# Kernel tuning notes

Measured on AMD Instinct MI355X. Metric: run time of the kernel, lower is better.

## Reference

```python
import jax, jax.numpy as jnp
import numpy as np

B, S, D = 16, 2048, 2048  # S == D required for m_q + output broadcast in original code


def setup_inputs() -> dict:
    key = jax.random.key(0)
    ks = jax.random.split(key, 8)
    scale = 1.0 / np.sqrt(D)
    return {
        "hidden_list": jax.random.normal(ks[0], (B, S, D), dtype=jnp.float32),
        "m_q": jax.random.normal(ks[1], (D,), dtype=jnp.float32),
        "Wq": jax.random.normal(ks[2], (D, D), dtype=jnp.float32) * scale,
        "bq": jax.random.normal(ks[3], (D,), dtype=jnp.float32) * scale,
        "Wm": jax.random.normal(ks[4], (D, D), dtype=jnp.float32) * scale,
        "bm": jax.random.normal(ks[5], (D,), dtype=jnp.float32) * scale,
        "Wa": jax.random.normal(ks[6], (D, D), dtype=jnp.float32) * scale,
        "ba": jax.random.normal(ks[7], (D,), dtype=jnp.float32) * scale,
    }


def reference(hidden_list, m_q, Wq, bq, Wm, bm, Wa, ba):
    # hidden_list: [B, S, D]; m_q: [D]
    hq = jnp.tanh(jnp.einsum("bsd,ed->bse", hidden_list, Wq) + bq)      # [B,S,D]
    mq = jnp.tanh(Wm @ m_q + bm)                                        # [D]
    Sg = hq * mq                                                        # gated bilinear, [B,S,D]
    alpha = jax.nn.softmax(jnp.einsum("bsd,ed->bse", Sg, Wa) + ba, axis=-1)  # [B,S,D]
    output = jnp.sum(alpha * hidden_list, axis=-1)                      # [B,S]
    m_q_new = m_q + output                                              # broadcast [D]+[B,S] (S==D)
    return output, m_q_new
```

## Files before the change

kernel.cpp:

```cpp
#include <hip/hip_runtime.h>

typedef unsigned short u16;
typedef short bf16x8 __attribute__((ext_vector_type(8)));
typedef u16 u16x8 __attribute__((ext_vector_type(8)));
typedef float f32x4 __attribute__((ext_vector_type(4)));

__device__ __forceinline__ float bf2f(u16 u) {
    union { unsigned u; float f; } c; c.u = ((unsigned)u) << 16; return c.f;
}
__device__ __forceinline__ u16 f2bf(float f) {
    union { float f; unsigned u; } c; c.f = f;
    unsigned r = c.u + 0x7FFFu + ((c.u >> 16) & 1u);
    return (u16)(r >> 16);
}
__device__ __forceinline__ float tanh_fast(float x) {
    float e = __expf(2.0f * x);
    return 1.0f - 2.0f / (e + 1.0f);
}
__device__ __forceinline__ void gll16(const void* g, void* l) {
    __builtin_amdgcn_global_load_lds((const __attribute__((address_space(1))) void*)g,
                                     (__attribute__((address_space(3))) void*)l, 16, 0, 0);
}

#define BAR() do { __builtin_amdgcn_sched_barrier(0); __builtin_amdgcn_s_barrier(); \
                   __builtin_amdgcn_sched_barrier(0); } while (0)

__global__ __launch_bounds__(256) void cvt_f32_bf16(const float* __restrict__ src,
                                                    u16* __restrict__ dst, int n8) {
    int i = blockIdx.x * blockDim.x + threadIdx.x;
    int stride = gridDim.x * blockDim.x;
    for (; i < n8; i += stride) {
        const float4* s = (const float4*)(src + (size_t)i * 8);
        float4 a = s[0], b = s[1];
        u16x8 o;
        o[0] = f2bf(a.x); o[1] = f2bf(a.y); o[2] = f2bf(a.z); o[3] = f2bf(a.w);
        o[4] = f2bf(b.x); o[5] = f2bf(b.y); o[6] = f2bf(b.z); o[7] = f2bf(b.w);
        *(u16x8*)(dst + (size_t)i * 8) = o;
    }
}

__global__ __launch_bounds__(256) void mq_kernel(const float* __restrict__ Wm,
                                                 const float* __restrict__ q,
                                                 const float* __restrict__ bm,
                                                 float* __restrict__ mq, int D) {
    int w = threadIdx.x >> 6, l = threadIdx.x & 63;
    int e = blockIdx.x * 4 + w;
    const float* wp = Wm + (size_t)e * D;
    float s = 0.f;
    for (int j = 0; j < D; j += 256) {
        float4 wv = *(const float4*)(wp + j + l * 4);
        float4 qv = *(const float4*)(q + j + l * 4);
        s += wv.x * qv.x + wv.y * qv.y + wv.z * qv.z + wv.w * qv.w;
    }
    #pragma unroll
    for (int o = 32; o >= 1; o >>= 1) s += __shfl_xor(s, o);
    if (l == 0) mq[e] = tanh_fast(s + bm[e]);
}

template <int EPI>
__global__ __launch_bounds__(256, 2) void gemm8(const u16* __restrict__ A,
                                                const u16* __restrict__ B,
                                                const float* __restrict__ bias,
                                                const float* __restrict__ gate,
                                                u16* __restrict__ C,
                                                int M, int N, int K) {
    __shared__ u16 sh[32768];
    char* LDS = (char*)sh;
    const int K2 = K * 2;
    const int KT = K >> 6;

    const int tid = threadIdx.x;
    const int w = tid >> 6, l = tid & 63;
    const int wm = w >> 1, wn = w & 1;

    int orig = blockIdx.x + gridDim.x * blockIdx.y;
    int nwg = gridDim.x * gridDim.y;
    int id = ((nwg & 7) == 0) ? ((orig & 7) * (nwg >> 3) + (orig >> 3)) : orig;
    const int tileN = (id % gridDim.x) * 128;
    const int tileM = (id / gridDim.x) * 128;

    const int srow = tid >> 3;
    const int cc = ((tid & 7) ^ (srow & 7)) << 4;
    const char* srcA = (const char*)A + (size_t)(tileM + srow) * K2 + cc;
    const char* srcB = (const char*)B + (size_t)(tileN + srow) * K2 + cc;
    char* dstBase = LDS + tid * 16;
    const size_t rowStep = (size_t)32 * K2;

#define STG_A(tk) do { size_t go = (size_t)(tk) * 128; char* d = dstBase + (((tk) & 1) << 14); \
    gll16(srcA + go,               d);         gll16(srcA + go + rowStep,     d + 4096);       \
    gll16(srcA + go + 2 * rowStep, d + 8192);  gll16(srcA + go + 3 * rowStep, d + 12288); } while (0)
#define STG_B(tk) do { size_t go = (size_t)(tk) * 128; char* d = dstBase + 32768 + (((tk) & 1) << 14); \
    gll16(srcB + go,               d);         gll16(srcB + go + rowStep,     d + 4096);       \
    gll16(srcB + go + 2 * rowStep, d + 8192);  gll16(srcB + go + 3 * rowStep, d + 12288); } while (0)

    const int sw = l & 7;
    const int rowA = (wm * 64 + (l & 15)) * 128;
    const int rowB = (wn * 64 + (l & 15)) * 128;
    const int ck0 = (((l >> 4) ^ sw) << 4);
    const int ck1 = (((4 + (l >> 4)) ^ sw) << 4);
    const char* pA0 = LDS + rowA + ck0;
    const char* pA1 = LDS + rowA + ck1;
    const char* pB0 = LDS + 32768 + rowB + ck0;
    const char* pB1 = LDS + 32768 + rowB + ck1;

    f32x4 acc[4][4] = {};

    STG_A(0); STG_B(0); STG_A(1); STG_B(1);
    asm volatile("s_waitcnt vmcnt(8)" ::: "memory");
    BAR();

#define ITER(t, P) do {                                                         \
    constexpr int SA = (P) * 16384;                                             \
    bf16x8 af[4][2], bf[4][2];                                                  \
               \
    _Pragma("unroll")                                                           \
    for (int fm = 0; fm < 4; ++fm) {                                            \
        af[fm][0] = *(const bf16x8*)(pA0 + SA + fm * 2048);                     \
        af[fm][1] = *(const bf16x8*)(pA1 + SA + fm * 2048);                     \
    }                                                                           \
    _Pragma("unroll")                                                           \
    for (int fn = 0; fn < 4; ++fn) {                                            \
        bf[fn][0] = *(const bf16x8*)(pB0 + SA + fn * 2048);                     \
        bf[fn][1] = *(const bf16x8*)(pB1 + SA + fn * 2048);                     \
    }                                                                           \
    asm volatile("s_waitcnt lgkmcnt(0)" ::: "memory");                          \
    __builtin_amdgcn_sched_barrier(0);                                          \
    BAR();                                                                      \
                \
    if ((t) + 2 < KT) { STG_A((t) + 2); STG_B((t) + 2); }                       \
    __builtin_amdgcn_s_setprio(1);                                              \
    _Pragma("unroll")                                                           \
    for (int fm = 0; fm < 4; ++fm)                                              \
        _Pragma("unroll")                                                       \
        for (int fn = 0; fn < 4; ++fn) {                                        \
            acc[fm][fn] = __builtin_amdgcn_mfma_f32_16x16x32_bf16(              \
                af[fm][0], bf[fn][0], acc[fm][fn], 0, 0, 0);                    \
            acc[fm][fn] = __builtin_amdgcn_mfma_f32_16x16x32_bf16(              \
                af[fm][1], bf[fn][1], acc[fm][fn], 0, 0, 0);                    \
        }                                                                       \
    __builtin_amdgcn_s_setprio(0);                                              \
    if ((t) + 2 < KT)      asm volatile("s_waitcnt vmcnt(8)" ::: "memory");     \
    else if ((t) + 1 < KT) asm volatile("s_waitcnt vmcnt(0)" ::: "memory");     \
    BAR();                                                                      \
} while (0)

    for (int tt = 0; tt < KT; tt += 2) {
        ITER(tt, 0);
        ITER(tt + 1, 1);
    }
#undef ITER
#undef STG_A
#undef STG_B

    const int cr = (l >> 4) * 4;
    const int cl = l & 15;
    #pragma unroll
    for (int fn = 0; fn < 4; ++fn) {
        const int col = tileN + wn * 64 + fn * 16 + cl;
        const float bs = bias[col];
        float gt = 0.f;
        if (EPI == 0) gt = gate[col];
        #pragma unroll
        for (int fm = 0; fm < 4; ++fm)
            #pragma unroll
            for (int r = 0; r < 4; ++r) {
                const int row = tileM + wm * 64 + fm * 16 + cr + r;
                float v = acc[fm][fn][r] + bs;
                if (EPI == 0) v = tanh_fast(v) * gt;
                C[(size_t)row * N + col] = f2bf(v);
            }
    }
}

__global__ __launch_bounds__(256) void softmax_out(const u16* __restrict__ logits,
                                                   const float* __restrict__ hidden,
                                                   const float* __restrict__ m_q,
                                                   float* __restrict__ out,
                                                   int D, int R) {
    const int r = blockIdx.x;
    const int t = threadIdx.x;
    const int w = t >> 6, l = t & 63;
    const u16* lp = logits + (size_t)r * D + t * 8;
    const float* hp = hidden + (size_t)r * D + t * 8;

    bf16x8 lv = *(const bf16x8*)lp;
    float lf[8];
    #pragma unroll
    for (int j = 0; j < 8; ++j) lf[j] = bf2f((u16)lv[j]);
    float4 h0 = *(const float4*)hp;
    float4 h1 = *(const float4*)(hp + 4);
    float hv[8] = {h0.x, h0.y, h0.z, h0.w, h1.x, h1.y, h1.z, h1.w};

    float m = lf[0];
    #pragma unroll
    for (int j = 1; j < 8; ++j) m = fmaxf(m, lf[j]);
    #pragma unroll
    for (int o = 32; o >= 1; o >>= 1) m = fmaxf(m, __shfl_xor(m, o));

    __shared__ float red[8];
    if (l == 0) red[w] = m;
    __syncthreads();
    m = fmaxf(fmaxf(red[0], red[1]), fmaxf(red[2], red[3]));
    __syncthreads();

    float se = 0.f, sh = 0.f;
    #pragma unroll
    for (int j = 0; j < 8; ++j) {
        float e = __expf(lf[j] - m);
        se += e;
        sh += e * hv[j];
    }
    #pragma unroll
    for (int o = 32; o >= 1; o >>= 1) { se += __shfl_xor(se, o); sh += __shfl_xor(sh, o); }
    if (l == 0) { red[w] = se; red[4 + w] = sh; }
    __syncthreads();
    if (t == 0) {
        float SE = red[0] + red[1] + red[2] + red[3];
        float SH = red[4] + red[5] + red[6] + red[7];
        float o = SH / SE;
        out[r] = o;
        out[R + r] = m_q[r & (D - 1)] + o;
    }
}

extern "C" void kernel_launch(void* const* d_in, const int* in_sizes, int n_in,
                              void* d_out, int out_size, void* d_ws, size_t ws_size,
                              hipStream_t stream) {
    const float* hidden = (const float*)d_in[0];
    const float* m_q    = (const float*)d_in[1];
    const float* Wq     = (const float*)d_in[2];
    const float* bq     = (const float*)d_in[3];
    const float* Wm     = (const float*)d_in[4];
    const float* bm     = (const float*)d_in[5];
    const float* Wa     = (const float*)d_in[6];
    const float* ba     = (const float*)d_in[7];
    float* out = (float*)d_out;

    const int D = 2048;
    const int M = 16 * 2048;

    char* ws = (char*)d_ws;
    size_t oH  = 0;
    size_t oS  = oH  + (size_t)M * D * 2;
    size_t oWq = oS  + (size_t)M * D * 2;
    size_t oWa = oWq + (size_t)D * D * 2;
    size_t oMq = oWa + (size_t)D * D * 2;
    size_t need = oMq + (size_t)D * sizeof(float);
    if (ws_size < need) return;

    u16* hbf    = (u16*)(ws + oH);
    u16* Sg     = (u16*)(ws + oS);
    u16* Wqb    = (u16*)(ws + oWq);
    u16* Wab    = (u16*)(ws + oWa);
    float* mq   = (float*)(ws + oMq);
    u16* logits = hbf;

    cvt_f32_bf16<<<4096, 256, 0, stream>>>(hidden, hbf, M * D / 8);
    cvt_f32_bf16<<<1024, 256, 0, stream>>>(Wq, Wqb, D * D / 8);
    cvt_f32_bf16<<<1024, 256, 0, stream>>>(Wa, Wab, D * D / 8);
    mq_kernel<<<D / 4, 256, 0, stream>>>(Wm, m_q, bm, mq, D);

    dim3 grid(D / 128, M / 128);
    gemm8<0><<<grid, 256, 0, stream>>>(hbf, Wqb, bq, mq, Sg, M, D, D);
    gemm8<1><<<grid, 256, 0, stream>>>(Sg, Wab, ba, nullptr, logits, M, D, D);

    softmax_out<<<M, 256, 0, stream>>>(logits, hidden, m_q, out, D, M);
}
```

Before: 763.5 us.

## Enlarge GEMM tiles to 256x256 with 8 waves and a 4-stage LDS ring

Replaces the 128x128, 4-wave bf16 GEMM with a 256x256 tile computed by 512 threads (2x4 waves, each wave owning 128x64). K steps drop to 32 and a four-buffer LDS ring is used. Because each buffer is only rewritten two iterations later, the pre-MFMA barrier and explicit lgkmcnt wait are removed, leaving one barrier per K step. The intent is more data reuse per byte loaded and less synchronisation. In exchange, 128KB of LDS limits occupancy to one block per CU and adds accumulator register pressure.

```diff
diff --git a/kernel.cpp b/kernel.cpp
--- a/kernel.cpp
+++ b/kernel.cpp
@@ -22,8 +22,7 @@
                                      (__attribute__((address_space(3))) void*)l, 16, 0, 0);
 }
 
-#define BAR() do { __builtin_amdgcn_sched_barrier(0); __builtin_amdgcn_s_barrier(); \
-                   __builtin_amdgcn_sched_barrier(0); } while (0)
+#define BAR() __builtin_amdgcn_s_barrier()
 
 __global__ __launch_bounds__(256) void cvt_f32_bf16(const float* __restrict__ src,
                                                     u16* __restrict__ dst, int n8) {
@@ -58,99 +57,87 @@
 }
 
 template <int EPI>
-__global__ __launch_bounds__(256, 2) void gemm8(const u16* __restrict__ A,
-                                                const u16* __restrict__ B,
-                                                const float* __restrict__ bias,
-                                                const float* __restrict__ gate,
-                                                u16* __restrict__ C,
-                                                int M, int N, int K) {
-    __shared__ u16 sh[32768];
+__global__ __launch_bounds__(512, 2) void gemm_1b(const u16* __restrict__ A,
+                                                  const u16* __restrict__ B,
+                                                  const float* __restrict__ bias,
+                                                  const float* __restrict__ gate,
+                                                  u16* __restrict__ C,
+                                                  int M, int N, int K) {
+    __shared__ u16 sh[65536];
     char* LDS = (char*)sh;
     const int K2 = K * 2;
-    const int KT = K >> 6;
+    const int KT = K >> 5;
 
     const int tid = threadIdx.x;
     const int w = tid >> 6, l = tid & 63;
-    const int wm = w >> 1, wn = w & 1;
+    const int wm = w >> 2, wn = w & 3;
 
     int orig = blockIdx.x + gridDim.x * blockIdx.y;
     int nwg = gridDim.x * gridDim.y;
     int id = ((nwg & 7) == 0) ? ((orig & 7) * (nwg >> 3) + (orig >> 3)) : orig;
-    const int tileN = (id % gridDim.x) * 128;
-    const int tileM = (id / gridDim.x) * 128;
-
-    const int srow = tid >> 3;
-    const int cc = ((tid & 7) ^ (srow & 7)) << 4;
-    const char* srcA = (const char*)A + (size_t)(tileM + srow) * K2 + cc;
-    const char* srcB = (const char*)B + (size_t)(tileN + srow) * K2 + cc;
-    char* dstBase = LDS + tid * 16;
-    const size_t rowStep = (size_t)32 * K2;
-
-#define STG_A(tk) do { size_t go = (size_t)(tk) * 128; char* d = dstBase + (((tk) & 1) << 14); \
-    gll16(srcA + go,               d);         gll16(srcA + go + rowStep,     d + 4096);       \
-    gll16(srcA + go + 2 * rowStep, d + 8192);  gll16(srcA + go + 3 * rowStep, d + 12288); } while (0)
-#define STG_B(tk) do { size_t go = (size_t)(tk) * 128; char* d = dstBase + 32768 + (((tk) & 1) << 14); \
-    gll16(srcB + go,               d);         gll16(srcB + go + rowStep,     d + 4096);       \
-    gll16(srcB + go + 2 * rowStep, d + 8192);  gll16(srcB + go + 3 * rowStep, d + 12288); } while (0)
-
-    const int sw = l & 7;
-    const int rowA = (wm * 64 + (l & 15)) * 128;
-    const int rowB = (wn * 64 + (l & 15)) * 128;
-    const int ck0 = (((l >> 4) ^ sw) << 4);
-    const int ck1 = (((4 + (l >> 4)) ^ sw) << 4);
-    const char* pA0 = LDS + rowA + ck0;
-    const char* pA1 = LDS + rowA + ck1;
-    const char* pB0 = LDS + 32768 + rowB + ck0;
-    const char* pB1 = LDS + 32768 + rowB + ck1;
-
-    f32x4 acc[4][4] = {};
-
-    STG_A(0); STG_B(0); STG_A(1); STG_B(1);
-    asm volatile("s_waitcnt vmcnt(8)" ::: "memory");
+    const int tileN = (id % gridDim.x) * 256;
+    const int tileM = (id / gridDim.x) * 256;
+
+    const int e_sw = (l & 7) ^ (l >> 3);
+    const int r_lane = 2 * (l >> 3) + (e_sw >> 2);
+    const int c_lane = (e_sw & 3) << 4;
+    const int ch0 = w * 2, ch1 = w * 2 + 1;
+    const char* sA0 = (const char*)A + (size_t)(tileM + ch0 * 16 + r_lane) * K2 + c_lane;
+    const char* sA1 = (const char*)A + (size_t)(tileM + ch1 * 16 + r_lane) * K2 + c_lane;
+    const char* sB0 = (const char*)B + (size_t)(tileN + ch0 * 16 + r_lane) * K2 + c_lane;
+    const char* sB1 = (const char*)B + (size_t)(tileN + ch1 * 16 + r_lane) * K2 + c_lane;
+    char* dA0 = LDS + ch0 * 1024;
+    char* dA1 = LDS + ch1 * 1024;
+    char* dB0 = LDS + 65536 + ch0 * 1024;
+    char* dB1 = LDS + 65536 + ch1 * 1024;
+
+#define STG(tk, SB) do { size_t go = (size_t)(tk) * 64;                         \
+    gll16(sA0 + go, dA0 + (SB)); gll16(sA1 + go, dA1 + (SB));                   \
+    gll16(sB0 + go, dB0 + (SB)); gll16(sB1 + go, dB1 + (SB)); } while (0)
+
+    const int prd = ((l & 15) >> 1) * 128 +
+                    ((((l & 1) << 2) | (l >> 4)) ^ ((l & 15) >> 1)) * 16;
+    const char* pRA = LDS + wm * 8192 + prd;
+    const char* pRB = LDS + 65536 + wn * 4096 + prd;
+
+    f32x4 acc[8][4] = {};
+
+    STG(0, 0); STG(1, 16384);
+    asm volatile("s_waitcnt vmcnt(4)" ::: "memory");
     BAR();
 
 #define ITER(t, P) do {                                                         \
-    constexpr int SA = (P) * 16384;                                             \
-    bf16x8 af[4][2], bf[4][2];                                                  \
-               \
+    constexpr int SL = (P) * 16384;                                             \
+    constexpr int SN = (((P) + 2) & 3) * 16384;                                 \
+    bf16x8 af[8], bf[4];                                                        \
     _Pragma("unroll")                                                           \
-    for (int fm = 0; fm < 4; ++fm) {                                            \
-        af[fm][0] = *(const bf16x8*)(pA0 + SA + fm * 2048);                     \
-        af[fm][1] = *(const bf16x8*)(pA1 + SA + fm * 2048);                     \
-    }                                                                           \
+    for (int fm = 0; fm < 8; ++fm)                                              \
+        af[fm] = *(const bf16x8*)(pRA + SL + fm * 1024);                        \
     _Pragma("unroll")                                                           \
-    for (int fn = 0; fn < 4; ++fn) {                                            \
-        bf[fn][0] = *(const bf16x8*)(pB0 + SA + fn * 2048);                     \
-        bf[fn][1] = *(const bf16x8*)(pB1 + SA + fn * 2048);                     \
-    }                                                                           \
-    asm volatile("s_waitcnt lgkmcnt(0)" ::: "memory");                          \
-    __builtin_amdgcn_sched_barrier(0);                                          \
-    BAR();                                                                      \
-                \
-    if ((t) + 2 < KT) { STG_A((t) + 2); STG_B((t) + 2); }                       \
+    for (int fn = 0; fn < 4; ++fn)                                              \
+        bf[fn] = *(const bf16x8*)(pRB + SL + fn * 1024);                        \
+    if ((t) + 2 < KT) STG((t) + 2, SN);                                         \
     __builtin_amdgcn_s_setprio(1);                                              \
     _Pragma("unroll")                                                           \
-    for (int fm = 0; fm < 4; ++fm)                                              \
+    for (int fm = 0; fm < 8; ++fm)                                              \
         _Pragma("unroll")                                                       \
-        for (int fn = 0; fn < 4; ++fn) {                                        \
+        for (int fn = 0; fn < 4; ++fn)                                          \
             acc[fm][fn] = __builtin_amdgcn_mfma_f32_16x16x32_bf16(              \
-                af[fm][0], bf[fn][0], acc[fm][fn], 0, 0, 0);                    \
-            acc[fm][fn] = __builtin_amdgcn_mfma_f32_16x16x32_bf16(              \
-                af[fm][1], bf[fn][1], acc[fm][fn], 0, 0, 0);                    \
-        }                                                                       \
+                af[fm], bf[fn], acc[fm][fn], 0, 0, 0);                          \
     __builtin_amdgcn_s_setprio(0);                                              \
-    if ((t) + 2 < KT)      asm volatile("s_waitcnt vmcnt(8)" ::: "memory");     \
-    else if ((t) + 1 < KT) asm volatile("s_waitcnt vmcnt(0)" ::: "memory");     \
+    if ((t) + 2 < KT) asm volatile("s_waitcnt vmcnt(4)" ::: "memory");          \
+    else              asm volatile("s_waitcnt vmcnt(0)" ::: "memory");          \
     BAR();                                                                      \
 } while (0)
 
-    for (int tt = 0; tt < KT; tt += 2) {
+    for (int tt = 0; tt < KT; tt += 4) {
         ITER(tt, 0);
         ITER(tt + 1, 1);
+        ITER(tt + 2, 2);
+        ITER(tt + 3, 3);
     }
 #undef ITER
-#undef STG_A
-#undef STG_B
+#undef STG
 
     const int cr = (l >> 4) * 4;
     const int cl = l & 15;
@@ -161,10 +148,10 @@
         float gt = 0.f;
         if (EPI == 0) gt = gate[col];
         #pragma unroll
-        for (int fm = 0; fm < 4; ++fm)
+        for (int fm = 0; fm < 8; ++fm)
             #pragma unroll
             for (int r = 0; r < 4; ++r) {
-                const int row = tileM + wm * 64 + fm * 16 + cr + r;
+                const int row = tileM + wm * 128 + fm * 16 + cr + r;
                 float v = acc[fm][fn][r] + bs;
                 if (EPI == 0) v = tanh_fast(v) * gt;
                 C[(size_t)row * N + col] = f2bf(v);
@@ -260,9 +247,9 @@
     cvt_f32_bf16<<<1024, 256, 0, stream>>>(Wa, Wab, D * D / 8);
     mq_kernel<<<D / 4, 256, 0, stream>>>(Wm, m_q, bm, mq, D);
 
-    dim3 grid(D / 128, M / 128);
-    gemm8<0><<<grid, 256, 0, stream>>>(hbf, Wqb, bq, mq, Sg, M, D, D);
-    gemm8<1><<<grid, 256, 0, stream>>>(Sg, Wab, ba, nullptr, logits, M, D, D);
+    dim3 grid(D / 256, M / 256);
+    gemm_1b<0><<<grid, 512, 0, stream>>>(hbf, Wqb, bq, mq, Sg, M, D, D);
+    gemm_1b<1><<<grid, 512, 0, stream>>>(Sg, Wab, ba, nullptr, logits, M, D, D);
 
     softmax_out<<<M, 256, 0, stream>>>(logits, hidden, m_q, out, D, M);
 }
```

After: 692.1 us. 1.1x faster.
